# Kernel tuning notes

Measured on AMD Instinct MI355X. Metric: run time of the kernel, lower is better.

Reference implementation:

```python
import jax, jax.numpy as jnp
import numpy as np

NUM_HEADS = 32
NUM_KV_HEADS = 8
HEAD_DIM = 128
ROPE_THETA = 10000.0
HIDDEN = NUM_HEADS * HEAD_DIM


def setup_inputs() -> dict:
    key = jax.random.key(0)
    ks = jax.random.split(key, 5)
    B, S = 2, 2048
    hidden_states = jax.random.normal(ks[0], (B, S, HIDDEN), dtype=jnp.float32)
    wq = jax.random.normal(ks[1], (HIDDEN, HIDDEN), dtype=jnp.float32) * 0.02
    wk = jax.random.normal(ks[2], (NUM_KV_HEADS * HEAD_DIM, HIDDEN), dtype=jnp.float32) * 0.02
    wv = jax.random.normal(ks[3], (NUM_KV_HEADS * HEAD_DIM, HIDDEN), dtype=jnp.float32) * 0.02
    wo = jax.random.normal(ks[4], (HIDDEN, HIDDEN), dtype=jnp.float32) * 0.02
    position_ids = jnp.broadcast_to(jnp.arange(S, dtype=jnp.int64 if jax.config.read('jax_enable_x64') else jnp.int32)[None, :], (B, S))
    return {"hidden_states": hidden_states, "position_ids": position_ids,
            "wq": wq, "wk": wk, "wv": wv, "wo": wo}


def _rotate_half(x):
    x1, x2 = jnp.split(x, 2, axis=-1)
    return jnp.concatenate((-x2, x1), axis=-1)


def _rope_tables(position_ids, dtype):
    # inv_freq: [head_dim/2]
    inv_freq = 1.0 / (ROPE_THETA ** (jnp.arange(0, HEAD_DIM, 2, dtype=jnp.float32) / HEAD_DIM))
    # freqs per position: [B, S, head_dim/2] -> emb [B, S, head_dim]
    freqs = position_ids.astype(jnp.float32)[..., None] * inv_freq  # bsd2
    emb = jnp.concatenate((freqs, freqs), axis=-1)
    # unsqueeze head dim -> [B, 1, S, head_dim]
    return jnp.cos(emb).astype(dtype)[:, None], jnp.sin(emb).astype(dtype)[:, None]


def reference(hidden_states, position_ids, wq, wk, wv, wo):
    B, S, H = hidden_states.shape
    n_rep = NUM_HEADS // NUM_KV_HEADS
    # projections (torch Linear: x @ W^T)
    q = (hidden_states @ wq.T).reshape(B, S, NUM_HEADS, HEAD_DIM).transpose(0, 2, 1, 3)
    k = (hidden_states @ wk.T).reshape(B, S, NUM_KV_HEADS, HEAD_DIM).transpose(0, 2, 1, 3)
    v = (hidden_states @ wv.T).reshape(B, S, NUM_KV_HEADS, HEAD_DIM).transpose(0, 2, 1, 3)
    cos, sin = _rope_tables(position_ids, hidden_states.dtype)
    q = q * cos + _rotate_half(q) * sin
    k = k * cos + _rotate_half(k) * sin
    # repeat_kv: [B, kvH, S, D] -> [B, H, S, D]
    k = jnp.repeat(k, n_rep, axis=1)
    v = jnp.repeat(v, n_rep, axis=1)
    scale = 1.0 / jnp.sqrt(jnp.asarray(HEAD_DIM, dtype=hidden_states.dtype))
    scores = jnp.einsum('bhqd,bhkd->bhqk', q, k) * scale
    causal = jnp.tril(jnp.ones((S, S), dtype=bool))
    scores = jnp.where(causal[None, None], scores, jnp.finfo(scores.dtype).min)
    # softmax in fp32 then cast back (matches HF upcast)
    attn = jax.nn.softmax(scores.astype(jnp.float32), axis=-1).astype(q.dtype)
    out = jnp.einsum('bhqk,bhkd->bhqd', attn, v)
    out = out.transpose(0, 2, 1, 3).reshape(B, S, H)
    return out @ wo.T
```

## Files before the change

### kernel.cpp

```cpp
#include <hip/hip_runtime.h>
#include <stdint.h>

#define NH      32
#define NKVH    8
#define HD      128
#define BATCH   2
#define SEQ     2048
#define HIDDEN  4096
#define KVDIM   1024
#define TOKENS  (BATCH*SEQ)

typedef __bf16 bf16x8 __attribute__((ext_vector_type(8)));
typedef float  f32x4  __attribute__((ext_vector_type(4)));

__device__ __forceinline__ uint16_t f32_to_bf16(float f) {
  union { float f; uint32_t u; } v; v.f = f;
  uint32_t r = v.u + 0x7FFFu + ((v.u >> 16) & 1u);
  return (uint16_t)(r >> 16);
}
__device__ __forceinline__ float bf16_to_f32(uint16_t h) {
  union { uint32_t u; float f; } v; v.u = ((uint32_t)h) << 16;
  return v.f;
}
__device__ __forceinline__ bf16x8 ld_frag(const uint16_t* p) {
  return *(const bf16x8*)p;
}
#define MFMA_BF16(a,b,c) __builtin_amdgcn_mfma_f32_16x16x32_bf16((a),(b),(c),0,0,0)
#define NEG_BIG (-1.0e30f)

typedef __attribute__((address_space(1))) void as1_void;
typedef __attribute__((address_space(3))) void as3_void;
__device__ __forceinline__ void gload_lds16(const void* g, void* l) {
  __builtin_amdgcn_global_load_lds((as1_void*)g, (as3_void*)l, 16, 0, 0);
}

__device__ __forceinline__ void cvt8(const float* __restrict__ s,
                                     uint16_t* __restrict__ d, size_t i) {
  const float4* sp = (const float4*)s + 2*i;
  float4 a = sp[0], b = sp[1];
  union { uint16_t u[8]; uint4 v; } o;
  o.u[0]=f32_to_bf16(a.x); o.u[1]=f32_to_bf16(a.y);
  o.u[2]=f32_to_bf16(a.z); o.u[3]=f32_to_bf16(a.w);
  o.u[4]=f32_to_bf16(b.x); o.u[5]=f32_to_bf16(b.y);
  o.u[6]=f32_to_bf16(b.z); o.u[7]=f32_to_bf16(b.w);
  ((uint4*)d)[i] = o.v;
}

__global__ __launch_bounds__(256) void cvt_all(
    const float* __restrict__ X,  const float* __restrict__ Wq,
    const float* __restrict__ Wk, const float* __restrict__ Wv,
    uint16_t* __restrict__ R0, uint16_t* __restrict__ R1,
    uint16_t* __restrict__ R2, uint16_t* __restrict__ R3)
{
  int blk = blockIdx.x;
  const float* s; uint16_t* d; int b0;
  if (blk < 8192)       { s = X;  d = R0; b0 = 0; }
  else if (blk < 16384) { s = Wq; d = R1; b0 = 8192; }
  else if (blk < 18432) { s = Wk; d = R2; b0 = 16384; }
  else                  { s = Wv; d = R3; b0 = 18432; }
  cvt8(s, d, (size_t)(blk - b0)*256 + threadIdx.x);
}

__global__ __launch_bounds__(256) void cvt_one(
    const float* __restrict__ s, uint16_t* __restrict__ d)
{
  cvt8(s, d, (size_t)blockIdx.x*256 + threadIdx.x);
}

#define BKG   32
#define NBUF  4

__device__ __forceinline__ void store_c(uint16_t* p, float v) { *p = f32_to_bf16(v); }
__device__ __forceinline__ void store_c(float*    p, float v) { *p = v; }

template <int IF, typename TC>
__device__ __forceinline__ void gemm_body256(
    const uint16_t* __restrict__ A, const uint16_t* __restrict__ B,
    TC* __restrict__ C, int m0, int n0, int N, int K)
{
  constexpr int BM     = IF * 32;
  constexpr int AINSTS = BM / 128;
  __shared__ __align__(16) uint16_t As[NBUF][BM  * BKG];
  __shared__ __align__(16) uint16_t Bs[NBUF][256 * BKG];

  const int tid  = threadIdx.x;
  const int wave = tid >> 6;
  const int lane = tid & 63;
  const int wm = wave >> 2;
  const int wn = wave & 3;
  const int fr = lane & 15;
  const int fo = (lane >> 4) * 8;

  const int srow = tid >> 2;
  const int scol = (tid & 3) * 8;
  const uint16_t* Ag = A + (size_t)(m0 + srow) * K + scol;
  const uint16_t* Bg = B + (size_t)(n0 + srow) * K + scol;
  const int wuo = wave * 16 * BKG;

  const int NT = K / BKG;

  #pragma unroll
  for (int t = 0; t < 3; ++t) {
    #pragma unroll
    for (int a = 0; a < AINSTS; ++a)
      gload_lds16(Ag + (size_t)a*128*K + t*BKG, &As[t][a*128*BKG + wuo]);
    gload_lds16(Bg + t*BKG,                  &Bs[t][wuo]);
    gload_lds16(Bg + (size_t)128*K + t*BKG,  &Bs[t][128*BKG + wuo]);
  }

  f32x4 acc[IF][4] = {};

  for (int t = 0; t < NT; ++t) {
    if (t + 3 <= NT) {
      if constexpr (IF == 8) asm volatile("s_waitcnt vmcnt(8)" ::: "memory");
      else                   asm volatile("s_waitcnt vmcnt(6)" ::: "memory");
    } else if (t + 2 <= NT) {
      if constexpr (IF == 8) asm volatile("s_waitcnt vmcnt(4)" ::: "memory");
      else                   asm volatile("s_waitcnt vmcnt(3)" ::: "memory");
    } else {
      asm volatile("s_waitcnt vmcnt(0)" ::: "memory");
    }
    __builtin_amdgcn_s_barrier();
    asm volatile("" ::: "memory");

    if (t + 3 < NT) {
      const int s = (t + 3) & (NBUF - 1);
      #pragma unroll
      for (int a = 0; a < AINSTS; ++a)
        gload_lds16(Ag + (size_t)a*128*K + (t+3)*BKG, &As[s][a*128*BKG + wuo]);
      gload_lds16(Bg + (t+3)*BKG,                 &Bs[s][wuo]);
      gload_lds16(Bg + (size_t)128*K + (t+3)*BKG, &Bs[s][128*BKG + wuo]);
    }

    const int cb = t & (NBUF - 1);
    const uint16_t* Asb = &As[cb][(wm * (BM/2)) * BKG];
    const uint16_t* Bsb = &Bs[cb][(wn * 64) * BKG];
    bf16x8 bfj[4], afi[IF];
    #pragma unroll
    for (int j = 0; j < 4; ++j)  bfj[j] = ld_frag(&Bsb[(j*16 + fr)*BKG + fo]);
    #pragma unroll
    for (int i = 0; i < IF; ++i) afi[i] = ld_frag(&Asb[(i*16 + fr)*BKG + fo]);
    __builtin_amdgcn_s_setprio(1);
    #pragma unroll
    for (int i = 0; i < IF; ++i)
      #pragma unroll
      for (int j = 0; j < 4; ++j)
        acc[i][j] = MFMA_BF16(afi[i], bfj[j], acc[i][j]);
    __builtin_amdgcn_s_setprio(0);
  }

  const int cr = (lane >> 4) * 4;
  #pragma unroll
  for (int i = 0; i < IF; ++i)
    #pragma unroll
    for (int j = 0; j < 4; ++j)
      #pragma unroll
      for (int r = 0; r < 4; ++r)
        store_c(&C[(size_t)(m0 + wm*(BM/2) + i*16 + cr + r) * N
                   + (n0 + wn*64 + j*16 + fr)],
                acc[i][j][r]);
}

__global__ __launch_bounds__(512, 2) void qkv_gemm(
    const uint16_t* __restrict__ X,
    const uint16_t* __restrict__ Wq, const uint16_t* __restrict__ Wk,
    const uint16_t* __restrict__ Wv,
    uint16_t* __restrict__ Qo, uint16_t* __restrict__ Ko, uint16_t* __restrict__ Vo)
{
  int bx = blockIdx.x;
  const uint16_t* Bm; uint16_t* Cm; int n0, N;
  if (bx < 16)      { Bm = Wq; Cm = Qo; n0 = bx*256;      N = HIDDEN; }
  else if (bx < 20) { Bm = Wk; Cm = Ko; n0 = (bx-16)*256; N = KVDIM;  }
  else              { Bm = Wv; Cm = Vo; n0 = (bx-20)*256; N = KVDIM;  }
  gemm_body256<4, uint16_t>(X, Bm, Cm, blockIdx.y*128, n0, N, HIDDEN);
}

__global__ __launch_bounds__(512, 2) void out_gemm(
    const uint16_t* __restrict__ A, const uint16_t* __restrict__ B,
    float* __restrict__ C, int N, int K)
{
  gemm_body256<8, float>(A, B, C, blockIdx.y*256, blockIdx.x*256, N, K);
}

__global__ __launch_bounds__(256) void rope_kernel(
    uint16_t* __restrict__ Q, uint16_t* __restrict__ K)
{
  int idx = blockIdx.x * 256 + threadIdx.x;
  int j = idx & 63;
  int rest = idx >> 6;
  int h = rest % (NH + NKVH);
  int t = rest / (NH + NKVH);
  float pos = (float)(t % SEQ);
  float inv_freq = __exp10f(-0.0625f * (float)j);
  float ang = pos * inv_freq;
  float s, c;
  __sincosf(ang, &s, &c);
  uint16_t* base = (h < NH) ? (Q + (size_t)t*HIDDEN + h*HD)
                            : (K + (size_t)t*KVDIM + (h-NH)*HD);
  float x1 = bf16_to_f32(base[j]);
  float x2 = bf16_to_f32(base[j+64]);
  base[j]    = f32_to_bf16(x1*c - x2*s);
  base[j+64] = f32_to_bf16(x2*c + x1*s);
}

__global__ __launch_bounds__(256) void transpose_v(
    const uint16_t* __restrict__ V, uint16_t* __restrict__ Vt)
{
  __shared__ uint16_t tile[64][66];
  int bh = blockIdx.z;  int b = bh >> 3, h = bh & 7;
  int s0 = blockIdx.x * 64;
  int d0 = blockIdx.y * 64;
  int tx = threadIdx.x & 63;
  int ty = threadIdx.x >> 6;
  const uint16_t* Vp = V + (size_t)b*SEQ*KVDIM + (size_t)h*HD;
  for (int r = ty; r < 64; r += 4)
    tile[r][tx] = Vp[(size_t)(s0 + r)*KVDIM + d0 + tx];
  __syncthreads();
  uint16_t* Vtp = Vt + ((size_t)b*NKVH + h)*HD*SEQ;
  for (int r = ty; r < 64; r += 4)
    Vtp[(size_t)(d0 + r)*SEQ + s0 + tx] = tile[tx][r];
}

#define KSTR 136
#define VSTR 72

__global__ __launch_bounds__(256, 4) void flash_attn(
    uint16_t* __restrict__ Q, const uint16_t* __restrict__ K,
    const uint16_t* __restrict__ Vt)
{
  __shared__ __align__(16) uint16_t Ks[64*KSTR];
  __shared__ __align__(16) uint16_t Vs[128*VSTR];
  uint16_t* Ps = Ks;

  const int tid  = threadIdx.x;
  const int wave = tid >> 6;
  const int lane = tid & 63;
  const int fr = lane & 15;
  const int g  = lane >> 4;
  const int fo = g * 8;
  const int bh = blockIdx.y;
  const int b = bh >> 5, h = bh & 31;
  const int kvh = h >> 2;

  uint16_t*       Qh = Q  + (size_t)b*SEQ*HIDDEN + (size_t)h*HD;
  const uint16_t* Kp = K  + (size_t)b*SEQ*KVDIM  + (size_t)kvh*HD;
  const uint16_t* Vp = Vt + ((size_t)b*NKVH + kvh)*HD*SEQ;

  #pragma unroll
  for (int pass = 0; pass < 2; ++pass) {
    const int qt = pass ? (31 - (int)blockIdx.x) : (int)blockIdx.x;
    const int q0 = qt * 64;
    const int qrow_base = q0 + wave*16 + g*4;

    bf16x8 qf[4];
    #pragma unroll
    for (int ks = 0; ks < 4; ++ks)
      qf[ks] = ld_frag(Qh + (size_t)(q0 + wave*16 + fr)*HIDDEN + ks*32 + fo);

    float m_i[4], l_i[4];
    f32x4 oacc[8] = {};
    #pragma unroll
    for (int r = 0; r < 4; ++r) { m_i[r] = NEG_BIG; l_i[r] = 0.f; }

    const int nkt = qt + 1;
    for (int kt = 0; kt < nkt; ++kt) {
      const int k0 = kt * 64;
      __syncthreads();
      #pragma unroll
      for (int i = 0; i < 4; ++i) {
        int gi = tid + i*256;
        int kr = gi >> 4, kc = (gi & 15) * 8;
        *(bf16x8*)&Ks[kr*KSTR + kc] = *(const bf16x8*)(Kp + (size_t)(k0 + kr)*KVDIM + kc);
        int vr = gi >> 3, vc = (gi & 7) * 8;
        *(bf16x8*)&Vs[vr*VSTR + vc] = *(const bf16x8*)(Vp + (size_t)vr*SEQ + k0 + vc);
      }
      __syncthreads();

      f32x4 sacc[4] = {};
      #pragma unroll
      for (int ks = 0; ks < 4; ++ks) {
        bf16x8 bk[4];
        #pragma unroll
        for (int j = 0; j < 4; ++j) bk[j] = ld_frag(&Ks[(j*16 + fr)*KSTR + ks*32 + fo]);
        #pragma unroll
        for (int j = 0; j < 4; ++j) sacc[j] = MFMA_BF16(qf[ks], bk[j], sacc[j]);
      }

      const bool diag = (kt == qt);
      #pragma unroll
      for (int r = 0; r < 4; ++r) {
        float vals[4];
        #pragma unroll
        for (int j = 0; j < 4; ++j) {
          float v = sacc[j][r] * 0.08838834764831845f;
          if (diag && (k0 + j*16 + fr > qrow_base + r)) v = NEG_BIG;
          vals[j] = v;
        }
        float mt = fmaxf(fmaxf(vals[0], vals[1]), fmaxf(vals[2], vals[3]));
        #pragma unroll
        for (int off = 1; off < 16; off <<= 1) mt = fmaxf(mt, __shfl_xor(mt, off, 64));
        float mn = fmaxf(m_i[r], mt);
        float alpha = __expf(fminf(m_i[r] - mn, 0.f));
        float lt = 0.f;
        #pragma unroll
        for (int j = 0; j < 4; ++j) {
          float p = __expf(fminf(vals[j] - mn, 0.f));
          sacc[j][r] = p;
          lt += p;
        }
        #pragma unroll
        for (int off = 1; off < 16; off <<= 1) lt += __shfl_xor(lt, off, 64);
        m_i[r] = mn;
        l_i[r] = l_i[r]*alpha + lt;
        #pragma unroll
        for (int n = 0; n < 8; ++n) oacc[n][r] *= alpha;
      }

      __syncthreads();

      #pragma unroll
      for (int j = 0; j < 4; ++j)
        #pragma unroll
        for (int r = 0; r < 4; ++r)
          Ps[(wave*16 + g*4 + r)*VSTR + j*16 + fr] = f32_to_bf16(sacc[j][r]);

      #pragma unroll
      for (int ks = 0; ks < 2; ++ks) {
        bf16x8 ap = ld_frag(&Ps[(wave*16 + fr)*VSTR + ks*32 + fo]);
        #pragma unroll
        for (int half = 0; half < 2; ++half) {
          bf16x8 bv[4];
          #pragma unroll
          for (int n = 0; n < 4; ++n)
            bv[n] = ld_frag(&Vs[((half*4 + n)*16 + fr)*VSTR + ks*32 + fo]);
          #pragma unroll
          for (int n = 0; n < 4; ++n)
            oacc[half*4 + n] = MFMA_BF16(ap, bv[n], oacc[half*4 + n]);
        }
      }
    }

    #pragma unroll
    for (int r = 0; r < 4; ++r) {
      float inv_l = 1.0f / l_i[r];
      #pragma unroll
      for (int n = 0; n < 8; ++n)
        Qh[(size_t)(qrow_base + r)*HIDDEN + n*16 + fr] = f32_to_bf16(oacc[n][r] * inv_l);
    }
    __syncthreads();
  }
}

extern "C" void kernel_launch(void* const* d_in, const int* in_sizes, int n_in,
                              void* d_out, int out_size, void* d_ws, size_t ws_size,
                              hipStream_t stream)
{
  (void)in_sizes; (void)n_in; (void)out_size; (void)ws_size;
  const float* hidden = (const float*)d_in[0];
  const float* wq = (const float*)d_in[2];
  const float* wk = (const float*)d_in[3];
  const float* wv = (const float*)d_in[4];
  const float* wo = (const float*)d_in[5];
  float* out = (float*)d_out;

  uint16_t* R0 = (uint16_t*)d_ws;
  uint16_t* R1 = R0 + (size_t)HIDDEN*HIDDEN;
  uint16_t* R2 = R1 + (size_t)HIDDEN*HIDDEN;
  uint16_t* R3 = R2 + (size_t)KVDIM*HIDDEN;
  uint16_t* Qb = R3 + (size_t)KVDIM*HIDDEN;
  uint16_t* Kb = Qb + (size_t)TOKENS*HIDDEN;
  uint16_t* Vb = Kb + (size_t)TOKENS*KVDIM;

  dim3 blk(256);
  dim3 blk512(512);
  cvt_all<<<dim3(20480), blk, 0, stream>>>(hidden, wq, wk, wv, R0, R1, R2, R3);
  qkv_gemm<<<dim3(24, TOKENS/128), blk512, 0, stream>>>(R0, R1, R2, R3, Qb, Kb, Vb);
  rope_kernel<<<dim3(TOKENS*(NH+NKVH)*64/256), blk, 0, stream>>>(Qb, Kb);
  cvt_one<<<dim3(HIDDEN*HIDDEN/8/256), blk, 0, stream>>>(wo, R0);
  transpose_v<<<dim3(SEQ/64, HD/64, BATCH*NKVH), blk, 0, stream>>>(Vb, R1);
  flash_attn<<<dim3(16, BATCH*NH), blk, 0, stream>>>(Qb, Kb, R1);
  out_gemm<<<dim3(HIDDEN/256, TOKENS/256), blk512, 0, stream>>>(Qb, R0, out, HIDDEN, HIDDEN);
}
```

Before: 906.8 us.

## Shrink GEMM tiles to 128x128 with 256 threads and 3-stage pipeline

```diff
diff --git a/kernel.cpp b/kernel.cpp
--- a/kernel.cpp
+++ b/kernel.cpp
@@ -67,119 +67,103 @@
   cvt8(s, d, (size_t)blockIdx.x*256 + threadIdx.x);
 }
 
-#define BKG   32
-#define NBUF  4
-
 __device__ __forceinline__ void store_c(uint16_t* p, float v) { *p = f32_to_bf16(v); }
 __device__ __forceinline__ void store_c(float*    p, float v) { *p = v; }
 
-template <int IF, typename TC>
-__device__ __forceinline__ void gemm_body256(
+template <typename TC>
+__device__ __forceinline__ void gemm_body(
     const uint16_t* __restrict__ A, const uint16_t* __restrict__ B,
     TC* __restrict__ C, int m0, int n0, int N, int K)
 {
-  constexpr int BM     = IF * 32;
-  constexpr int AINSTS = BM / 128;
-  __shared__ __align__(16) uint16_t As[NBUF][BM  * BKG];
-  __shared__ __align__(16) uint16_t Bs[NBUF][256 * BKG];
-
+  __shared__ __align__(16) uint16_t As[3][128*32];
+  __shared__ __align__(16) uint16_t Bs[3][128*32];
   const int tid  = threadIdx.x;
   const int wave = tid >> 6;
   const int lane = tid & 63;
-  const int wm = wave >> 2;
-  const int wn = wave & 3;
+  const int wm = (wave >> 1) * 64;
+  const int wn = (wave & 1) * 64;
+  const int srow = lane >> 2;
+  const int scol = (lane & 3) * 8;
+  const uint16_t* Ap = A + (size_t)(m0 + wave*16 + srow) * K + scol;
+  const uint16_t* Bp = B + (size_t)(n0 + wave*16 + srow) * K + scol;
+  const int wuo = wave*16*32;
   const int fr = lane & 15;
   const int fo = (lane >> 4) * 8;
-
-  const int srow = tid >> 2;
-  const int scol = (tid & 3) * 8;
-  const uint16_t* Ag = A + (size_t)(m0 + srow) * K + scol;
-  const uint16_t* Bg = B + (size_t)(n0 + srow) * K + scol;
-  const int wuo = wave * 16 * BKG;
-
-  const int NT = K / BKG;
+  const int NT = K / 32;
 
   #pragma unroll
-  for (int t = 0; t < 3; ++t) {
-    #pragma unroll
-    for (int a = 0; a < AINSTS; ++a)
-      gload_lds16(Ag + (size_t)a*128*K + t*BKG, &As[t][a*128*BKG + wuo]);
-    gload_lds16(Bg + t*BKG,                  &Bs[t][wuo]);
-    gload_lds16(Bg + (size_t)128*K + t*BKG,  &Bs[t][128*BKG + wuo]);
+  for (int t = 0; t < 2; ++t) {
+    gload_lds16(Ap + (size_t)t*32,                &As[t][wuo]);
+    gload_lds16(Ap + (size_t)64*K + (size_t)t*32, &As[t][64*32 + wuo]);
+    gload_lds16(Bp + (size_t)t*32,                &Bs[t][wuo]);
+    gload_lds16(Bp + (size_t)64*K + (size_t)t*32, &Bs[t][64*32 + wuo]);
   }
 
-  f32x4 acc[IF][4] = {};
-
+  f32x4 acc[4][4] = {};
+  int s_cur = 0, s_stage = 2;
   for (int t = 0; t < NT; ++t) {
-    if (t + 3 <= NT) {
-      if constexpr (IF == 8) asm volatile("s_waitcnt vmcnt(8)" ::: "memory");
-      else                   asm volatile("s_waitcnt vmcnt(6)" ::: "memory");
-    } else if (t + 2 <= NT) {
-      if constexpr (IF == 8) asm volatile("s_waitcnt vmcnt(4)" ::: "memory");
-      else                   asm volatile("s_waitcnt vmcnt(3)" ::: "memory");
-    } else {
-      asm volatile("s_waitcnt vmcnt(0)" ::: "memory");
-    }
+    if (t < NT - 1) asm volatile("s_waitcnt vmcnt(4)" ::: "memory");
+    else            asm volatile("s_waitcnt vmcnt(0)" ::: "memory");
     __builtin_amdgcn_s_barrier();
     asm volatile("" ::: "memory");
 
-    if (t + 3 < NT) {
-      const int s = (t + 3) & (NBUF - 1);
-      #pragma unroll
-      for (int a = 0; a < AINSTS; ++a)
-        gload_lds16(Ag + (size_t)a*128*K + (t+3)*BKG, &As[s][a*128*BKG + wuo]);
-      gload_lds16(Bg + (t+3)*BKG,                 &Bs[s][wuo]);
-      gload_lds16(Bg + (size_t)128*K + (t+3)*BKG, &Bs[s][128*BKG + wuo]);
+    if (t + 2 < NT) {
+      const size_t k2 = (size_t)(t + 2) * 32;
+      gload_lds16(Ap + k2,                &As[s_stage][wuo]);
+      gload_lds16(Ap + (size_t)64*K + k2, &As[s_stage][64*32 + wuo]);
+      gload_lds16(Bp + k2,                &Bs[s_stage][wuo]);
+      gload_lds16(Bp + (size_t)64*K + k2, &Bs[s_stage][64*32 + wuo]);
     }
 
-    const int cb = t & (NBUF - 1);
-    const uint16_t* Asb = &As[cb][(wm * (BM/2)) * BKG];
-    const uint16_t* Bsb = &Bs[cb][(wn * 64) * BKG];
-    bf16x8 bfj[4], afi[IF];
-    #pragma unroll
-    for (int j = 0; j < 4; ++j)  bfj[j] = ld_frag(&Bsb[(j*16 + fr)*BKG + fo]);
-    #pragma unroll
-    for (int i = 0; i < IF; ++i) afi[i] = ld_frag(&Asb[(i*16 + fr)*BKG + fo]);
+    const uint16_t* Asb = As[s_cur];
+    const uint16_t* Bsb = Bs[s_cur];
+    bf16x8 af[4], bfr[4];
+    #pragma unroll
+    for (int i = 0; i < 4; ++i) af[i]  = ld_frag(&Asb[(wm + i*16 + fr)*32 + fo]);
+    #pragma unroll
+    for (int j = 0; j < 4; ++j) bfr[j] = ld_frag(&Bsb[(wn + j*16 + fr)*32 + fo]);
     __builtin_amdgcn_s_setprio(1);
     #pragma unroll
-    for (int i = 0; i < IF; ++i)
+    for (int i = 0; i < 4; ++i)
       #pragma unroll
       for (int j = 0; j < 4; ++j)
-        acc[i][j] = MFMA_BF16(afi[i], bfj[j], acc[i][j]);
+        acc[i][j] = MFMA_BF16(af[i], bfr[j], acc[i][j]);
     __builtin_amdgcn_s_setprio(0);
+
+    s_cur   = (s_cur   == 2) ? 0 : s_cur + 1;
+    s_stage = (s_stage == 2) ? 0 : s_stage + 1;
   }
 
   const int cr = (lane >> 4) * 4;
   #pragma unroll
-  for (int i = 0; i < IF; ++i)
+  for (int i = 0; i < 4; ++i)
     #pragma unroll
     for (int j = 0; j < 4; ++j)
       #pragma unroll
       for (int r = 0; r < 4; ++r)
-        store_c(&C[(size_t)(m0 + wm*(BM/2) + i*16 + cr + r) * N
-                   + (n0 + wn*64 + j*16 + fr)],
+        store_c(&C[(size_t)(m0 + wm + i*16 + cr + r) * N + (n0 + wn + j*16 + fr)],
                 acc[i][j][r]);
 }
 
-__global__ __launch_bounds__(512, 2) void qkv_gemm(
+__global__ __launch_bounds__(256, 3) void qkv_gemm(
     const uint16_t* __restrict__ X,
     const uint16_t* __restrict__ Wq, const uint16_t* __restrict__ Wk,
     const uint16_t* __restrict__ Wv,
     uint16_t* __restrict__ Qo, uint16_t* __restrict__ Ko, uint16_t* __restrict__ Vo)
 {
   int bx = blockIdx.x;
-  const uint16_t* Bm; uint16_t* Cm; int n0, N;
-  if (bx < 16)      { Bm = Wq; Cm = Qo; n0 = bx*256;      N = HIDDEN; }
-  else if (bx < 20) { Bm = Wk; Cm = Ko; n0 = (bx-16)*256; N = KVDIM;  }
-  else              { Bm = Wv; Cm = Vo; n0 = (bx-20)*256; N = KVDIM;  }
-  gemm_body256<4, uint16_t>(X, Bm, Cm, blockIdx.y*128, n0, N, HIDDEN);
-}
-
-__global__ __launch_bounds__(512, 2) void out_gemm(
+  const uint16_t* B; uint16_t* C; int n0, N;
+  if (bx < 32)      { B = Wq; C = Qo; n0 = bx*128;      N = HIDDEN; }
+  else if (bx < 40) { B = Wk; C = Ko; n0 = (bx-32)*128; N = KVDIM;  }
+  else              { B = Wv; C = Vo; n0 = (bx-40)*128; N = KVDIM;  }
+  gemm_body<uint16_t>(X, B, C, blockIdx.y*128, n0, N, HIDDEN);
+}
+
+__global__ __launch_bounds__(256, 3) void out_gemm(
     const uint16_t* __restrict__ A, const uint16_t* __restrict__ B,
     float* __restrict__ C, int N, int K)
 {
-  gemm_body256<8, float>(A, B, C, blockIdx.y*256, blockIdx.x*256, N, K);
+  gemm_body<float>(A, B, C, blockIdx.y*128, blockIdx.x*128, N, K);
 }
 
 __global__ __launch_bounds__(256) void rope_kernel(
@@ -372,12 +356,11 @@
   uint16_t* Vb = Kb + (size_t)TOKENS*KVDIM;
 
   dim3 blk(256);
-  dim3 blk512(512);
   cvt_all<<<dim3(20480), blk, 0, stream>>>(hidden, wq, wk, wv, R0, R1, R2, R3);
-  qkv_gemm<<<dim3(24, TOKENS/128), blk512, 0, stream>>>(R0, R1, R2, R3, Qb, Kb, Vb);
+  qkv_gemm<<<dim3(48, TOKENS/128), blk, 0, stream>>>(R0, R1, R2, R3, Qb, Kb, Vb);
   rope_kernel<<<dim3(TOKENS*(NH+NKVH)*64/256), blk, 0, stream>>>(Qb, Kb);
   cvt_one<<<dim3(HIDDEN*HIDDEN/8/256), blk, 0, stream>>>(wo, R0);
   transpose_v<<<dim3(SEQ/64, HD/64, BATCH*NKVH), blk, 0, stream>>>(Vb, R1);
   flash_attn<<<dim3(16, BATCH*NH), blk, 0, stream>>>(Qb, Kb, R1);
-  out_gemm<<<dim3(HIDDEN/256, TOKENS/256), blk512, 0, stream>>>(Qb, R0, out, HIDDEN, HIDDEN);
-}
+  out_gemm<<<dim3(HIDDEN/128, TOKENS/128), blk, 0, stream>>>(Qb, R0, out, HIDDEN, HIDDEN);
+}
```

Measured after the change: 834.7 us. 8.0% less time.
